# Optimization experiments

Hardware: AMD Instinct MI355X
Metric: run time of the kernel (lower is better)

The kernel has to match this reference:

```python
import jax, jax.numpy as jnp
import numpy as np

B, NL, L1, D = 16, 12, 197, 768   # batch, num_layers, 1+num_patches, embed_dim
E, K, C, IMG = 4, 3, 21, 224      # num_experts, topk, num_classes, image_size


def setup_inputs() -> dict:
    key = jax.random.key(0)
    k0, k1, k2 = jax.random.split(key, 3)
    features = jax.random.normal(k0, (B, NL, L1, D), jnp.float32)
    gate_W = jax.random.normal(k1, (D, E), jnp.float32) / np.sqrt(D).astype(np.float32)
    gate_b = jnp.zeros((E,), jnp.float32)
    expert_W = jax.random.normal(k2, (E, D, C), jnp.float32) / np.sqrt(D).astype(np.float32)
    expert_b = jnp.zeros((E, C), jnp.float32)
    return dict(features=features, gate_W=gate_W, gate_b=gate_b,
                expert_W=expert_W, expert_b=expert_b)


def reference(features, gate_W, gate_b, expert_W, expert_b):
    cls_tokens = features[:, :, 0, :]          # [B, NL, D]
    feats = features[:, :, 1:, :]              # [B, NL, L, D]
    gate_score = cls_tokens @ gate_W + gate_b  # [B, NL, E]
    gate_prob = jax.nn.softmax(gate_score.transpose(0, 2, 1), axis=-1)  # [B, E, NL]
    # per-expert topk over layers (vectorized over experts)
    topv, topi = jax.lax.top_k(gate_prob, K)   # [B, E, K]
    # gather selected layer feature maps: [B, E, K, L, D]
    gathered = jnp.take_along_axis(feats[:, None], topi[:, :, :, None, None], axis=2)
    w = jax.nn.softmax(topv, axis=-1)          # re-softmax of topk values, [B, E, K]
    mixed = jnp.einsum('bek,bekld->beld', w, gathered)  # [B, E, L, D]
    # expert heads (UPerNet modeled as linear decode + bilinear upsample)
    logits = jnp.einsum('beld,edc->belc', mixed, expert_W) + expert_b[None, :, None, :]
    L = logits.shape[2]
    g = int(np.sqrt(L))                        # 14x14 patch grid
    logits = logits.reshape(B, E, g, g, C).transpose(0, 1, 4, 2, 3)  # [B,E,C,g,g]
    logits = jax.image.resize(logits, (B, E, C, IMG, IMG), method='bilinear')
    return logits.mean(axis=1)                 # mean over experts -> [B, C, IMG, IMG]
```

## Files before the change

kernel.cpp:

```cpp
#include <hip/hip_runtime.h>
#include <math.h>

#define B_ 16
#define NL_ 12
#define L1_ 197
#define D_ 768
#define E_ 4
#define K_ 3
#define C_ 21
#define IMG_ 224
#define LP_ 196
#define NJ_ 84
#define MT_ 52
#define KSTEPS 24

typedef __attribute__((ext_vector_type(8))) short short8;
typedef __attribute__((ext_vector_type(4))) float f32x4;
typedef unsigned short ushort_t;

__device__ __forceinline__ ushort_t bf16rne(float x) {
    unsigned u = __float_as_uint(x);
    unsigned r = (u + 0x7FFFu + ((u >> 16) & 1u)) >> 16;
    return (ushort_t)r;
}

__device__ __forceinline__ void select_be(const float* __restrict__ gs, int b, int e,
                                          int idx[3], float w[3]) {
    float p[NL_]; float mx = -1e30f;
    #pragma unroll
    for (int nl = 0; nl < NL_; ++nl) { float v = gs[(b * NL_ + nl) * E_ + e]; p[nl] = v; mx = fmaxf(mx, v); }
    float ss = 0.f;
    #pragma unroll
    for (int nl = 0; nl < NL_; ++nl) { p[nl] = expf(p[nl] - mx); ss += p[nl]; }
    float inv = 1.0f / ss;
    #pragma unroll
    for (int nl = 0; nl < NL_; ++nl) p[nl] *= inv;
    unsigned used = 0; float v[3];
    #pragma unroll
    for (int k = 0; k < 3; ++k) {
        float best = -1.f; int bi = 0;
        #pragma unroll
        for (int nl = 0; nl < NL_; ++nl)
            if (!((used >> nl) & 1u) && p[nl] > best) { best = p[nl]; bi = nl; }
        used |= 1u << bi; idx[k] = bi; v[k] = best;
    }
    float x1 = expf(v[1] - v[0]), x2 = expf(v[2] - v[0]);
    float isw = 1.0f / (1.0f + x1 + x2);
    w[0] = isw; w[1] = x1 * isw; w[2] = x2 * isw;
}

__global__ __launch_bounds__(256) void prep_kernel(
        const float* __restrict__ feat, const float* __restrict__ gW,
        const float* __restrict__ gb, const float* __restrict__ eW,
        ushort_t* __restrict__ WtB, float* __restrict__ gs) {
    int blk = blockIdx.x, t = threadIdx.x;
    if (blk < B_ * NL_) {
        if (t < 64) {
            const float* cls = feat + (size_t)blk * L1_ * D_;
            float a0 = 0.f, a1 = 0.f, a2 = 0.f, a3 = 0.f;
            for (int q = 0; q < D_ / 64; ++q) {
                int d = t + 64 * q;
                float x = cls[d];
                float4 w = *(const float4*)(gW + (size_t)d * E_);
                a0 += x * w.x; a1 += x * w.y; a2 += x * w.z; a3 += x * w.w;
            }
            for (int off = 32; off > 0; off >>= 1) {
                a0 += __shfl_down(a0, off); a1 += __shfl_down(a1, off);
                a2 += __shfl_down(a2, off); a3 += __shfl_down(a3, off);
            }
            if (t == 0) {
                gs[blk * E_ + 0] = a0 + gb[0]; gs[blk * E_ + 1] = a1 + gb[1];
                gs[blk * E_ + 2] = a2 + gb[2]; gs[blk * E_ + 3] = a3 + gb[3];
            }
        }
    } else {
        int j = blk - B_ * NL_;
        if (j < NJ_) {
            int e = j / C_, c = j % C_;
            for (int k = t; k < D_; k += 256)
                WtB[(size_t)j * D_ + k] = bf16rne(eW[((size_t)e * D_ + k) * C_ + c]);
        } else {
            for (int k = t; k < D_; k += 256) WtB[(size_t)j * D_ + k] = 0;
        }
    }
}

__global__ __launch_bounds__(256) void select_kernel(
        const float* __restrict__ gs, int* __restrict__ topi,
        float* __restrict__ wgt, int* __restrict__ flag) {
    __shared__ int sidx[B_ * E_ * 3];
    int t = threadIdx.x;
    if (t < B_ * E_) {
        int b = t >> 2, e = t & 3;
        int idx[3]; float w[3];
        select_be(gs, b, e, idx, w);
        #pragma unroll
        for (int k = 0; k < 3; ++k) {
            topi[t * 3 + k] = idx[k]; wgt[t * 3 + k] = w[k]; sidx[t * 3 + k] = idx[k];
        }
    }
    __syncthreads();
    if (t < B_ * NL_) {
        int b = t / NL_, nl = t % NL_;
        int f = 0;
        #pragma unroll
        for (int ek = 0; ek < 12; ++ek) f |= (sidx[b * 12 + ek] == nl);
        flag[t] = f;
    }
}

#define GLOAD(ks, A0, A1, W0v, W1v) do {                                        \
    int _k0 = (ks) * 32;                                                        \
    if (avalid) { const f32x4* _p = (const f32x4*)(arow_base + _k0);            \
                  A0 = _p[kg * 2]; A1 = _p[kg * 2 + 1]; }                       \
    W0v = *(const short8*)(brow0 + _k0 + kg * 8);                               \
    if (bvalid1) W1v = *(const short8*)(brow1 + _k0 + kg * 8);                  \
} while (0)

#define SSTORE(buf, A0, A1, W0v, W1v) do {                                      \
    short8 _av;                                                                 \
    _Pragma("unroll")                                                           \
    for (int _i = 0; _i < 4; ++_i) {                                            \
        _av[_i]     = (short)bf16rne(A0[_i]);                                   \
        _av[_i + 4] = (short)bf16rne(A1[_i]);                                   \
    }                                                                           \
    Ab[buf][r * 5 + aslotw] = _av;                                              \
    Bb[buf][r * 5 + aslotw] = W0v;                                              \
    if (bvalid1) Bb[buf][(64 + r) * 5 + aslotw] = W1v;                          \
} while (0)

#define COMPUTE(buf) do {                                                       \
    short8 _af = Ab[buf][aidx];                                                 \
    _Pragma("unroll")                                                           \
    for (int _nt = 0; _nt < 6; ++_nt)                                           \
        acc[_nt] = __builtin_amdgcn_mfma_f32_16x16x32_bf16(                     \
            _af, Bb[buf][bidx[_nt]], acc[_nt], 0, 0, 0);                        \
} while (0)

__global__ __launch_bounds__(256, 3) void gemm_kernel(
        const float* __restrict__ feat, const ushort_t* __restrict__ WtB,
        const int* __restrict__ flag, float* __restrict__ proj) {
    int blk = blockIdx.x;
    int tile = blk & 3;
    int bn = blk >> 2;
    if (flag[bn] == 0) return;
    int rows_real = min(MT_, LP_ - tile * MT_);

    __shared__ short8 Ab[2][64 * 5];
    __shared__ short8 Bb[2][96 * 5];

    int t = threadIdx.x;
    int w = t >> 6, lane = t & 63;
    int r = t >> 2, kg = t & 3;
    int aslotw = kg ^ (r & 3);
    bool avalid = r < rows_real;
    bool bvalid1 = t < 128;

    const float* arow_base = feat + ((size_t)bn * L1_ + 1 + tile * MT_ + r) * D_;
    const ushort_t* brow0 = WtB + (size_t)r * D_;
    const ushort_t* brow1 = WtB + (size_t)(64 + r) * D_;

    int arow = w * 16 + (lane & 15);
    int aidx = arow * 5 + ((lane >> 4) ^ (arow & 3));
    int bidx[6];
    #pragma unroll
    for (int nt = 0; nt < 6; ++nt) {
        int jr = nt * 16 + (lane & 15);
        bidx[nt] = jr * 5 + ((lane >> 4) ^ (jr & 3));
    }

    {
        f32x4 fa0 = {0,0,0,0}, fa1 = {0,0,0,0};
        short8 wb0 = (short8)0, wb1 = (short8)0;
        GLOAD(0, fa0, fa1, wb0, wb1);
        SSTORE(0, fa0, fa1, wb0, wb1);
    }
    __syncthreads();

    f32x4 acc[6];
    #pragma unroll
    for (int nt = 0; nt < 6; ++nt) acc[nt] = (f32x4)0.0f;

    for (int s = 0; s < KSTEPS; ++s) {
        int cur = s & 1;
        f32x4 fa0 = {0,0,0,0}, fa1 = {0,0,0,0};
        short8 wb0, wb1;
        if (s + 1 < KSTEPS) GLOAD(s + 1, fa0, fa1, wb0, wb1);
        COMPUTE(cur);
        if (s + 1 < KSTEPS) SSTORE(cur ^ 1, fa0, fa1, wb0, wb1);
        __syncthreads();
    }

    int lr = w * 16 + ((lane >> 4) << 2);
    int l0 = tile * MT_ + lr;
    if (lr < MT_ && l0 < LP_) {
        #pragma unroll
        for (int nt = 0; nt < 6; ++nt) {
            int j = nt * 16 + (lane & 15);
            if (j < NJ_)
                *(f32x4*)(proj + ((size_t)bn * NJ_ + j) * LP_ + l0) = acc[nt];
        }
    }
}

__global__ __launch_bounds__(256) void upsample_kernel(
        const float* __restrict__ proj, const int* __restrict__ topi,
        const float* __restrict__ wgt, const float* __restrict__ eb,
        float* __restrict__ out) {
    int bq = blockIdx.x;
    int q = bq & 7;
    int bc = bq >> 3;
    int b = bc / C_, c = bc % C_;
    int t = threadIdx.x;
    __shared__ float s[LP_];
    if (t < LP_) {
        float a = 0.25f * (eb[c] + eb[C_ + c] + eb[2 * C_ + c] + eb[3 * C_ + c]);
        #pragma unroll
        for (int e = 0; e < E_; ++e) {
            int base = (b * E_ + e) * 3;
            #pragma unroll
            for (int k = 0; k < 3; ++k) {
                int nl = topi[base + k];
                float wv = 0.25f * wgt[base + k];
                a += wv * proj[(((size_t)b * NL_ + nl) * NJ_ + e * C_ + c) * LP_ + t];
            }
        }
        s[t] = a;
    }
    __syncthreads();
    f32x4* out4 = (f32x4*)out + (size_t)bc * IMG_ * (IMG_ / 4);
    for (int i = t; i < 28 * 56; i += 256) {
        int oy = q * 28 + i / 56;
        int ox4 = (i % 56) * 4;
        float fy = (oy + 0.5f) * 0.0625f - 0.5f;
        fy = fminf(fmaxf(fy, 0.0f), 13.0f);
        int y0 = (int)fy;
        float ty = fy - (float)y0;
        int y1 = min(y0 + 1, 13);
        const float* r0 = s + y0 * 14;
        const float* r1 = s + y1 * 14;
        f32x4 res;
        #pragma unroll
        for (int u = 0; u < 4; ++u) {
            int ox = ox4 + u;
            float fx = (ox + 0.5f) * 0.0625f - 0.5f;
            fx = fminf(fmaxf(fx, 0.0f), 13.0f);
            int x0 = (int)fx;
            float tx = fx - (float)x0;
            int x1 = min(x0 + 1, 13);
            float v00 = r0[x0], v01 = r0[x1];
            float v10 = r1[x0], v11 = r1[x1];
            float top = v00 + tx * (v01 - v00);
            float bot = v10 + tx * (v11 - v10);
            res[u] = top + ty * (bot - top);
        }
        __builtin_nontemporal_store(res, &out4[oy * 56 + (i % 56)]);
    }
}

extern "C" void kernel_launch(void* const* d_in, const int* in_sizes, int n_in,
                              void* d_out, int out_size, void* d_ws, size_t ws_size,
                              hipStream_t stream) {
    const float* feat = (const float*)d_in[0];
    const float* gW   = (const float*)d_in[1];
    const float* gb   = (const float*)d_in[2];
    const float* eW   = (const float*)d_in[3];
    const float* eb   = (const float*)d_in[4];
    float* out = (float*)d_out;

    float* ws = (float*)d_ws;
    float*    gs   = ws;
    int*      topi = (int*)(ws + 768);
    float*    wgt  = ws + 960;
    int*      flag = (int*)(ws + 1152);
    ushort_t* WtB  = (ushort_t*)(ws + 1536);
    float*    proj = ws + 38400;

    hipLaunchKernelGGL(prep_kernel, dim3(B_ * NL_ + 96), dim3(256), 0, stream,
                       feat, gW, gb, eW, WtB, gs);
    hipLaunchKernelGGL(select_kernel, dim3(1), dim3(256), 0, stream,
                       gs, topi, wgt, flag);
    hipLaunchKernelGGL(gemm_kernel, dim3(B_ * NL_ * 4), dim3(256), 0, stream,
                       feat, WtB, flag, proj);
    hipLaunchKernelGGL(upsample_kernel, dim3(B_ * C_ * 8), dim3(256), 0, stream,
                       proj, topi, wgt, eb, out);
}
```

Measured before the change: 52.60 us.

## Compact selected layers into a work list and deepen GEMM global-load prefetch

The select kernel now builds a compact list of the (batch, layer) pairs that some expert selected, plus their count. The GEMM maps active blocks onto that list so the working blocks sit in the low part of the grid, and the rest exit at once. The GEMM main loop is unrolled by two with two register sets, so global loads are issued two K-steps ahead of the MFMA work. This aims to hide load latency better, at the cost of more registers, and the list is built by one serial thread.

```diff
diff --git a/kernel.cpp b/kernel.cpp
--- a/kernel.cpp
+++ b/kernel.cpp
@@ -87,8 +87,9 @@
 
 __global__ __launch_bounds__(256) void select_kernel(
         const float* __restrict__ gs, int* __restrict__ topi,
-        float* __restrict__ wgt, int* __restrict__ flag) {
+        float* __restrict__ wgt, int* __restrict__ list, int* __restrict__ nsel) {
     __shared__ int sidx[B_ * E_ * 3];
+    __shared__ int sflag[B_ * NL_];
     int t = threadIdx.x;
     if (t < B_ * E_) {
         int b = t >> 2, e = t & 3;
@@ -105,7 +106,14 @@
         int f = 0;
         #pragma unroll
         for (int ek = 0; ek < 12; ++ek) f |= (sidx[b * 12 + ek] == nl);
-        flag[t] = f;
+        sflag[t] = f;
+    }
+    __syncthreads();
+    if (t == 0) {
+        int n = 0;
+        for (int bn = 0; bn < B_ * NL_; ++bn)
+            if (sflag[bn]) list[n++] = bn;
+        nsel[0] = n;
     }
 }
 
@@ -139,11 +147,12 @@
 
 __global__ __launch_bounds__(256, 3) void gemm_kernel(
         const float* __restrict__ feat, const ushort_t* __restrict__ WtB,
-        const int* __restrict__ flag, float* __restrict__ proj) {
+        const int* __restrict__ list, const int* __restrict__ nsel,
+        float* __restrict__ proj) {
     int blk = blockIdx.x;
+    if (blk >= nsel[0] * 4) return;
     int tile = blk & 3;
-    int bn = blk >> 2;
-    if (flag[bn] == 0) return;
+    int bn = list[blk >> 2];
     int rows_real = min(MT_, LP_ - tile * MT_);
 
     __shared__ short8 Ab[2][64 * 5];
@@ -169,25 +178,26 @@
         bidx[nt] = jr * 5 + ((lane >> 4) ^ (jr & 3));
     }
 
-    {
-        f32x4 fa0 = {0,0,0,0}, fa1 = {0,0,0,0};
-        short8 wb0 = (short8)0, wb1 = (short8)0;
-        GLOAD(0, fa0, fa1, wb0, wb1);
-        SSTORE(0, fa0, fa1, wb0, wb1);
-    }
+    f32x4 Xa0 = (f32x4)0.f, Xa1 = (f32x4)0.f, Ya0 = (f32x4)0.f, Ya1 = (f32x4)0.f;
+    short8 Xb0 = (short8)0, Xb1 = (short8)0, Yb0 = (short8)0, Yb1 = (short8)0;
+
+    GLOAD(0, Xa0, Xa1, Xb0, Xb1);
+    GLOAD(1, Ya0, Ya1, Yb0, Yb1);
+    SSTORE(0, Xa0, Xa1, Xb0, Xb1);
     __syncthreads();
 
     f32x4 acc[6];
     #pragma unroll
     for (int nt = 0; nt < 6; ++nt) acc[nt] = (f32x4)0.0f;
 
-    for (int s = 0; s < KSTEPS; ++s) {
-        int cur = s & 1;
-        f32x4 fa0 = {0,0,0,0}, fa1 = {0,0,0,0};
-        short8 wb0, wb1;
-        if (s + 1 < KSTEPS) GLOAD(s + 1, fa0, fa1, wb0, wb1);
-        COMPUTE(cur);
-        if (s + 1 < KSTEPS) SSTORE(cur ^ 1, fa0, fa1, wb0, wb1);
+    for (int s = 0; s < KSTEPS; s += 2) {
+        if (s + 2 < KSTEPS) GLOAD(s + 2, Xa0, Xa1, Xb0, Xb1);
+        COMPUTE(0);
+        SSTORE(1, Ya0, Ya1, Yb0, Yb1);
+        __syncthreads();
+        if (s + 3 < KSTEPS) GLOAD(s + 3, Ya0, Ya1, Yb0, Yb1);
+        COMPUTE(1);
+        if (s + 2 < KSTEPS) SSTORE(0, Xa0, Xa1, Xb0, Xb1);
         __syncthreads();
     }
 
@@ -272,16 +282,17 @@
     float*    gs   = ws;
     int*      topi = (int*)(ws + 768);
     float*    wgt  = ws + 960;
-    int*      flag = (int*)(ws + 1152);
+    int*      list = (int*)(ws + 1152);
+    int*      nsel = (int*)(ws + 1344);
     ushort_t* WtB  = (ushort_t*)(ws + 1536);
     float*    proj = ws + 38400;
 
     hipLaunchKernelGGL(prep_kernel, dim3(B_ * NL_ + 96), dim3(256), 0, stream,
                        feat, gW, gb, eW, WtB, gs);
     hipLaunchKernelGGL(select_kernel, dim3(1), dim3(256), 0, stream,
-                       gs, topi, wgt, flag);
+                       gs, topi, wgt, list, nsel);
     hipLaunchKernelGGL(gemm_kernel, dim3(B_ * NL_ * 4), dim3(256), 0, stream,
-                       feat, WtB, flag, proj);
+                       feat, WtB, list, nsel, proj);
     hipLaunchKernelGGL(upsample_kernel, dim3(B_ * C_ * 8), dim3(256), 0, stream,
                        proj, topi, wgt, eb, out);
 }
```

New measurement: 62.02 us. 17.9% more time.
